# Optimization experiments

Measured on AMD Instinct MI355X. Metric: run time of the kernel, lower is better.

## Reference

```python
import jax, jax.numpy as jnp
import numpy as np

N_NODES = 500000
N_EDGES = 16000000


def setup_inputs() -> dict:
    key = jax.random.key(0)
    ks = jax.random.split(key, 9)
    x = jax.random.normal(ks[0], (N_NODES, 15), dtype=jnp.float32)
    edge_index = jax.random.randint(ks[1], (2, N_EDGES), 0, N_NODES, dtype=jnp.int64)
    batch_index = jax.random.randint(ks[2], (N_NODES,), 0, 64, dtype=jnp.int64)
    def glorot(k, shape):
        lim = (6.0 / (shape[0] + shape[1])) ** 0.5
        return jax.random.uniform(k, shape, jnp.float32, -lim, lim)
    W1 = glorot(ks[3], (15, 15)); b1 = jnp.zeros((15,), jnp.float32)
    W2 = glorot(ks[4], (15, 15)); b2 = jnp.zeros((15,), jnp.float32)
    W3 = glorot(ks[5], (15, 4));  b3 = jnp.zeros((4,), jnp.float32)
    return {"x": x, "edge_index": edge_index, "batch_index": batch_index,
            "W1": W1, "b1": b1, "W2": W2, "b2": b2, "W3": W3, "b3": b3}


def _gcn_conv(x, W, b, src, dst, norm, n):
    # linear transform (tiny GEMM), then normalized scatter-add aggregation
    h = x @ W                                   # [N, out]
    msg = h[src] * norm[:, None]                # [E+N, out] gather + scale
    out = jax.ops.segment_sum(msg, dst, num_segments=n)
    return out + b


def reference(x, edge_index, batch_index, W1, b1, W2, b2, W3, b3):
    n = x.shape[0]
    loops = jnp.arange(n, dtype=edge_index.dtype)
    src = jnp.concatenate([edge_index[0], loops])   # self-loops appended
    dst = jnp.concatenate([edge_index[1], loops])
    # symmetric normalization D^-1/2 A D^-1/2 (deg over targets, incl. self-loops)
    deg = jax.ops.segment_sum(jnp.ones_like(dst, dtype=x.dtype), dst, num_segments=n)
    dis = jnp.where(deg > 0, jax.lax.rsqrt(deg), 0.0)
    norm = dis[src] * dis[dst]                      # [E+N]
    h = jax.nn.relu(_gcn_conv(x, W1, b1, src, dst, norm, n))
    h = jax.nn.relu(_gcn_conv(h, W2, b2, src, dst, norm, n))
    out = _gcn_conv(h, W3, b3, src, dst, norm, n)   # [N, 4]
    return out
```

## Files before the change

### kernel.cpp

```cpp
#include <hip/hip_runtime.h>
#include <hip/hip_fp16.h>


typedef unsigned int uint;
typedef unsigned short ushort;
typedef unsigned long long ull;

#define NBMAX 1024
#define BKN 512
#define BCAP 17408
#define SCAP 24576
#define PT_THREADS 512
#define PT_TILE 8192
#define NPART 8
#define BAR_STRIDE 528
#define BAR_LAYER (7 * BAR_STRIDE)

__global__ void k_init(uint* __restrict__ gcur, uint* __restrict__ bars) {
    int t = threadIdx.x;
    gcur[t] = (uint)t * BCAP;
    for (int i = t; i < 3 * BAR_LAYER; i += 1024) bars[i] = 0;
}

__global__ __launch_bounds__(PT_THREADS) void k_part(const int* __restrict__ src,
                                                     const int* __restrict__ dst, int E,
                                                     uint* __restrict__ gcur,
                                                     uint* __restrict__ bucketed) {
    __shared__ uint stage[PT_TILE];
    __shared__ ushort sbuck[PT_TILE];
    __shared__ uint hist[NBMAX], lofs[NBMAX], base[NBMAX];
    __shared__ uint tsum[PT_THREADS];
    int t = threadIdx.x;
    long long start = (long long)blockIdx.x * PT_TILE;
    int cnt = (int)min((long long)PT_TILE, (long long)E - start);

    hist[2 * t] = 0; hist[2 * t + 1] = 0;
    __syncthreads();
    uint myb[16], myr[16], mys[16];
#pragma unroll
    for (int k = 0; k < 16; ++k) {
        int idx = t + k * PT_THREADS;
        if (idx < cnt) {
            uint d = (uint)dst[start + idx];
            uint s = (uint)src[start + idx];
            uint b = d >> 9;
            myb[k] = b;
            mys[k] = s | ((d & 511u) << 19);
            myr[k] = atomicAdd(&hist[b], 1u);
        }
    }
    __syncthreads();
    uint h0 = hist[2 * t], h1 = hist[2 * t + 1];
    tsum[t] = h0 + h1;
    __syncthreads();
    for (int off = 1; off < PT_THREADS; off <<= 1) {
        uint x = (t >= off) ? tsum[t - off] : 0u;
        __syncthreads();
        tsum[t] += x;
        __syncthreads();
    }
    uint ex = tsum[t] - (h0 + h1);
    lofs[2 * t] = ex;
    lofs[2 * t + 1] = ex + h0;
    if (h0) base[2 * t] = atomicAdd(&gcur[2 * t], h0);
    if (h1) base[2 * t + 1] = atomicAdd(&gcur[2 * t + 1], h1);
    __syncthreads();
#pragma unroll
    for (int k = 0; k < 16; ++k) {
        int idx = t + k * PT_THREADS;
        if (idx < cnt) {
            uint pos = lofs[myb[k]] + myr[k];
            stage[pos] = mys[k];
            sbuck[pos] = (ushort)myb[k];
        }
    }
    __syncthreads();
#pragma unroll
    for (int k = 0; k < 16; ++k) {
        int idx = t + k * PT_THREADS;
        if (idx < cnt) {
            uint b = sbuck[idx];
            uint pos = base[b] + ((uint)idx - lofs[b]);
            if (pos < (uint)(b + 1) * BCAP) bucketed[pos] = stage[idx];
        }
    }
}

__global__ __launch_bounds__(512) void k_csr(const uint* __restrict__ bucketed,
                                             const uint* __restrict__ gcur,
                                             uint* __restrict__ rowp8,
                                             float* __restrict__ dis,
                                             int* __restrict__ srcS, int N) {
    __shared__ uint c[BKN * NPART];
    __shared__ uint tsum[512];
    __shared__ __align__(16) int stage[SCAP];
    int b = blockIdx.x, t = threadIdx.x;
    uint beg = (uint)b * BCAP;
    uint end = min(gcur[b], (uint)(b + 1) * BCAP);
    for (int i = t; i < BKN * NPART; i += 512) c[i] = 0;
    __syncthreads();
    for (uint e = beg + t; e < end; e += 512) {
        uint v = bucketed[e];
        uint key = (((v & 0x7ffffu) >> 16) << 9) | (v >> 19);
        atomicAdd(&c[key], 1u);
    }
    __syncthreads();
    {
        int node = (b << 9) + t;
        if (node < N) {
            uint deg = 0;
#pragma unroll
            for (int p = 0; p < NPART; ++p) deg += c[(p << 9) | t];
            dis[node] = rsqrtf((float)(deg + 1u));
        }
    }
    uint cnt[8], pad[8], ps = 0;
#pragma unroll
    for (int i = 0; i < 8; ++i) {
        cnt[i] = c[t * 8 + i];
        pad[i] = (cnt[i] + 3u) & ~3u;
        ps += pad[i];
    }
    __syncthreads();
    tsum[t] = ps;
    __syncthreads();
    for (int off = 1; off < 512; off <<= 1) {
        uint x = (t >= off) ? tsum[t - off] : 0u;
        __syncthreads();
        tsum[t] += x;
        __syncthreads();
    }
    uint tot = tsum[511];
    uint kb = tsum[t] - ps;
    uint slab = (uint)b * SCAP;
    int p = t >> 6, local0 = (t & 63) << 3;
    uint run = kb;
#pragma unroll
    for (int i = 0; i < 8; ++i) {
        uint st = run;
        rowp8[((uint)p << 19) + (uint)((b << 9) + local0 + i)] =
            (slab + st) | (cnt[i] << 25);
        c[t * 8 + i] = st;
        for (uint q = cnt[i]; q < pad[i]; ++q) {
            uint idx = st + q;
            if (idx < (uint)SCAP) stage[idx] = N;
            else srcS[slab + idx] = N;
        }
        run += pad[i];
    }
    __syncthreads();
    for (uint e = beg + t; e < end; e += 512) {
        uint v = bucketed[e];
        uint s = v & 0x7ffffu;
        uint key = ((s >> 16) << 9) | (v >> 19);
        uint idx = atomicAdd(&c[key], 1u);
        if (idx < (uint)SCAP) stage[idx] = (int)s;
        else srcS[slab + idx] = (int)s;
    }
    __syncthreads();
    uint capped = min(tot, (uint)SCAP);
    uint cap4 = capped & ~3u;
    for (uint i = t * 4; i < cap4; i += 512 * 4)
        *(int4*)(srcS + slab + i) = *(const int4*)(stage + i);
    if (t < (int)(capped & 3u)) srcS[slab + cap4 + t] = stage[cap4 + t];
}

__global__ void k_lin_first(const float* __restrict__ x, const float* __restrict__ W,
                            const float* __restrict__ dis, __half* __restrict__ A, int N) {
    int i = blockIdx.x * blockDim.x + threadIdx.x;
    if (i >= N) return;
    float in[15];
#pragma unroll
    for (int j = 0; j < 15; ++j) in[j] = x[i * 15 + j];
    float di = dis[i];
#pragma unroll
    for (int o = 0; o < 15; ++o) {
        float acc = 0.f;
#pragma unroll
        for (int j = 0; j < 15; ++j) acc = fmaf(in[j], W[j * 15 + o], acc);
        A[i * 16 + o] = __float2half(acc * di);
    }
    A[i * 16 + 15] = __float2half(0.f);
}

__device__ __forceinline__ void softbar(uint* __restrict__ bars, int phase, int nblk) {
    __syncthreads();
    if (threadIdx.x == 0) {
        uint* row = bars + phase * BAR_STRIDE;
        uint ngroups = ((uint)nblk + 31u) >> 5;
        uint g = (uint)blockIdx.x >> 5;
        uint gsz = min(32u, (uint)nblk - g * 32u);
        uint prev = atomicAdd(&row[16 + g * 16], 1u);
        if (prev + 1u == gsz) atomicAdd(&row[0], 1u);
        int spins = 0;
        while (spins < 2000) {
            uint v = __hip_atomic_load(&row[0], __ATOMIC_RELAXED,
                                       __HIP_MEMORY_SCOPE_AGENT);
            if (v >= ngroups) break;
            __builtin_amdgcn_s_sleep(8);
            ++spins;
        }
    }
    __syncthreads();
}

template <int TW>
__device__ __forceinline__ void load_row(const __half* __restrict__ tab, int node,
                                         float (&acc)[TW]) {
    if constexpr (TW == 16) {
        int4 w0 = *(const int4*)(tab + (size_t)node * 16);
        int4 w1 = *(const int4*)(tab + (size_t)node * 16 + 8);
        const __half2* h0 = (const __half2*)&w0;
        const __half2* h1 = (const __half2*)&w1;
#pragma unroll
        for (int u = 0; u < 4; ++u) {
            float2 f0 = __half22float2(h0[u]);
            float2 f1 = __half22float2(h1[u]);
            acc[2 * u] = f0.x;
            acc[2 * u + 1] = f0.y;
            acc[8 + 2 * u] = f1.x;
            acc[8 + 2 * u + 1] = f1.y;
        }
    } else {
        int2 w = *(const int2*)(tab + (size_t)node * 4);
        const __half2* h = (const __half2*)&w;
        float2 f0 = __half22float2(h[0]);
        float2 f1 = __half22float2(h[1]);
        acc[0] = f0.x; acc[1] = f0.y; acc[2] = f1.x; acc[3] = f1.y;
    }
}

template <int TW>
__device__ __forceinline__ void gather_seg(const __half* __restrict__ tab,
                                           const int* __restrict__ srcS,
                                           uint rv, float (&acc)[TW]) {
    uint cnt = rv >> 25;
    if (!cnt) return;
    uint e = rv & 0x1ffffffu;
    uint end4 = e + ((cnt + 3u) & ~3u);
    for (; e < end4; e += 4) {
        int4 s4 = *(const int4*)(srcS + e);
        if constexpr (TW == 16) {
            const int4* p0 = (const int4*)(tab + (size_t)s4.x * 16);
            const int4* p1 = (const int4*)(tab + (size_t)s4.y * 16);
            const int4* p2 = (const int4*)(tab + (size_t)s4.z * 16);
            const int4* p3 = (const int4*)(tab + (size_t)s4.w * 16);
            int4 r[8];
            r[0] = p0[0]; r[1] = p1[0]; r[2] = p2[0]; r[3] = p3[0];
            r[4] = p0[1]; r[5] = p1[1]; r[6] = p2[1]; r[7] = p3[1];
#pragma unroll
            for (int q = 0; q < 8; ++q) {
                const __half2* h2 = (const __half2*)&r[q];
                int base = (q >> 2) * 8;
#pragma unroll
                for (int u = 0; u < 4; ++u) {
                    float2 f = __half22float2(h2[u]);
                    acc[base + 2 * u] += f.x;
                    acc[base + 2 * u + 1] += f.y;
                }
            }
        } else {
            int2 r0 = *(const int2*)(tab + (size_t)s4.x * 4);
            int2 r1 = *(const int2*)(tab + (size_t)s4.y * 4);
            int2 r2 = *(const int2*)(tab + (size_t)s4.z * 4);
            int2 r3 = *(const int2*)(tab + (size_t)s4.w * 4);
            const __half2* h0 = (const __half2*)&r0;
            const __half2* h1 = (const __half2*)&r1;
            const __half2* h2 = (const __half2*)&r2;
            const __half2* h3 = (const __half2*)&r3;
#pragma unroll
            for (int u = 0; u < 2; ++u) {
                float2 f0 = __half22float2(h0[u]);
                float2 f1 = __half22float2(h1[u]);
                float2 f2 = __half22float2(h2[u]);
                float2 f3 = __half22float2(h3[u]);
                acc[2 * u] += (f0.x + f1.x) + (f2.x + f3.x);
                acc[2 * u + 1] += (f0.y + f1.y) + (f2.y + f3.y);
            }
        }
    }
}

template <int L>
__global__ __launch_bounds__(512, 8) void k_pull_res(
    const __half* __restrict__ tab, const int* __restrict__ srcS,
    const uint* __restrict__ rowp8, const float* __restrict__ dis,
    const float* __restrict__ Wm, const float* __restrict__ bias,
    void* __restrict__ outp, uint* __restrict__ bars, int nblk, int N) {
    constexpr int TW = (L == 3) ? 4 : 16;
    __shared__ float wl[240];
    int t = threadIdx.x;
    int node = (blockIdx.x << 9) + t;
    if constexpr (L == 1) {
        for (int i = t; i < 225; i += 512) wl[i] = Wm[i];
        if (t < 15) wl[225 + t] = bias[t];
    }
    if constexpr (L == 2) {
        for (int i = t; i < 60; i += 512) wl[i] = Wm[i];
        if (t < 15) wl[60 + t] = bias[t];
    }
    if constexpr (L == 3) {
        if (t < 4) wl[t] = bias[t];
    }
    __syncthreads();
    bool v = node < N;
    float a[TW];
    if (v) load_row<TW>(tab, node, a);
    uint rv = v ? rowp8[(uint)node] : 0u;
    for (int p = 0; p < NPART; ++p) {
        uint nv = 0u;
        if (p < NPART - 1) {
            uint pb = (uint)(p + 1) << 19;
            if (v) nv = rowp8[pb + (uint)node];
        }
        if (v) gather_seg<TW>(tab, srcS, rv, a);
        if (p < NPART - 1) softbar(bars, p, nblk);
        rv = nv;
    }
    if (!v) return;
    float di = dis[node];
    if constexpr (L == 3) {
        float4 o;
        o.x = a[0] * di + wl[0];
        o.y = a[1] * di + wl[1];
        o.z = a[2] * di + wl[2];
        o.w = a[3] * di + wl[3];
        *(float4*)((float*)outp + (size_t)node * 4) = o;
    } else {
        float h[15];
#pragma unroll
        for (int j = 0; j < 15; ++j) {
            float bj = (L == 1) ? wl[225 + j] : wl[60 + j];
            h[j] = fmaxf(a[j] * di + bj, 0.f);
        }
        if constexpr (L == 1) {
            float o[16];
            o[15] = 0.f;
#pragma unroll
            for (int j = 0; j < 15; ++j) {
                float s = 0.f;
#pragma unroll
                for (int k = 0; k < 15; ++k) s = fmaf(h[k], wl[k * 15 + j], s);
                o[j] = s * di;
            }
            __half2 ob[8];
#pragma unroll
            for (int j = 0; j < 8; ++j)
                ob[j] = __floats2half2_rn(o[2 * j], o[2 * j + 1]);
            *(int4*)((__half*)outp + (size_t)node * 16) = *(int4*)&ob[0];
            *(int4*)((__half*)outp + (size_t)node * 16 + 8) = *(int4*)&ob[4];
        } else {
            float o[4];
#pragma unroll
            for (int j = 0; j < 4; ++j) {
                float s = 0.f;
#pragma unroll
                for (int k = 0; k < 15; ++k) s = fmaf(h[k], wl[k * 4 + j], s);
                o[j] = s * di;
            }
            __half2 ob[2];
            ob[0] = __floats2half2_rn(o[0], o[1]);
            ob[1] = __floats2half2_rn(o[2], o[3]);
            *(float2*)((__half*)outp + (size_t)node * 4) = *(float2*)&ob[0];
        }
    }
}

extern "C" void kernel_launch(void* const* d_in, const int* in_sizes, int n_in,
                              void* d_out, int out_size, void* d_ws, size_t ws_size,
                              hipStream_t stream) {
    const float* x  = (const float*)d_in[0];
    const int*   ei = (const int*)d_in[1];
    const float* W1 = (const float*)d_in[3];
    const float* b1 = (const float*)d_in[4];
    const float* W2 = (const float*)d_in[5];
    const float* b2 = (const float*)d_in[6];
    const float* W3 = (const float*)d_in[7];
    const float* b3 = (const float*)d_in[8];
    float* out = (float*)d_out;

    const int N = in_sizes[0] / 15;
    const int E = in_sizes[1] / 2;
    const int* src = ei;
    const int* dst = ei + E;
    const int NBr = (N + BKN - 1) / BKN;
    const int PB  = NBr;

    char* ws = (char*)d_ws;
    auto align = [](size_t v) { return (v + 255) & ~(size_t)255; };
    size_t off = 0;
    uint* rowp8 = (uint*)(ws + off); off += align((size_t)NPART * (1u << 19) * 4);
    float* dis  = (float*)(ws + off); off += align((size_t)N * 4);
    uint* gcur  = (uint*)(ws + off); off += align((size_t)NBMAX * 4);
    uint* bars  = (uint*)(ws + off); off += align((size_t)3 * BAR_LAYER * 4);
    int*  srcS  = (int*)(ws + off);  off += align((size_t)NBMAX * SCAP * 4);
    char* slabY = ws + off;
    uint*   bucketed = (uint*)slabY;
    __half* Bp = (__half*)slabY;
    __half* Cp = (__half*)(slabY + align((size_t)(N + 1) * 16 * 2));
    off += align((size_t)NBMAX * BCAP * 4);
    __half* Ap = (__half*)(ws + off);

    const int nTiles = (E + PT_TILE - 1) / PT_TILE;
    const int nbN = (N + 255) / 256;

    k_init<<<1, 1024, 0, stream>>>(gcur, bars);
    k_part<<<nTiles, PT_THREADS, 0, stream>>>(src, dst, E, gcur, bucketed);
    k_csr<<<NBr, 512, 0, stream>>>(bucketed, gcur, rowp8, dis, srcS, N);

    k_lin_first<<<nbN, 256, 0, stream>>>(x, W1, dis, Ap, N);
    hipMemsetAsync(Ap + (size_t)N * 16, 0, 16 * 2, stream);
    hipMemsetAsync(Bp + (size_t)N * 16, 0, 16 * 2, stream);
    hipMemsetAsync(Cp + (size_t)N * 4, 0, 4 * 2, stream);

    k_pull_res<1><<<PB, 512, 0, stream>>>(Ap, srcS, rowp8, dis, W2, b1, Bp,
                                          bars + 0 * BAR_LAYER, PB, N);
    k_pull_res<2><<<PB, 512, 0, stream>>>(Bp, srcS, rowp8, dis, W3, b2, Cp,
                                          bars + 1 * BAR_LAYER, PB, N);
    k_pull_res<3><<<PB, 512, 0, stream>>>(Cp, srcS, rowp8, dis, nullptr, b3, out,
                                          bars + 2 * BAR_LAYER, PB, N);
}
```

Baseline: 928.5 us.

## Split 16-wide gather rows across thread pairs, recombine via shared memory

For layers 1 and 2, each thread now gathers one 8-half slice of the feature row for two nodes instead of the full 16-half row for one node, so thread pairs cooperate on a node. The two slices are staged in a padded shared-memory tile and recombined before the dense transform. This cuts per-thread registers and spreads the memory-level parallelism differently across lanes. In exchange it adds a 34 KB shared buffer, which may limit occupancy, plus an extra block barrier.

After: 926.7 us. Within noise of the previous version (-0.2%).

```diff
diff --git a/kernel.cpp b/kernel.cpp
--- a/kernel.cpp
+++ b/kernel.cpp
@@ -204,79 +204,72 @@
     __syncthreads();
 }
 
-template <int TW>
-__device__ __forceinline__ void load_row(const __half* __restrict__ tab, int node,
-                                         float (&acc)[TW]) {
-    if constexpr (TW == 16) {
-        int4 w0 = *(const int4*)(tab + (size_t)node * 16);
-        int4 w1 = *(const int4*)(tab + (size_t)node * 16 + 8);
-        const __half2* h0 = (const __half2*)&w0;
-        const __half2* h1 = (const __half2*)&w1;
-#pragma unroll
-        for (int u = 0; u < 4; ++u) {
-            float2 f0 = __half22float2(h0[u]);
-            float2 f1 = __half22float2(h1[u]);
-            acc[2 * u] = f0.x;
-            acc[2 * u + 1] = f0.y;
-            acc[8 + 2 * u] = f1.x;
-            acc[8 + 2 * u + 1] = f1.y;
-        }
-    } else {
-        int2 w = *(const int2*)(tab + (size_t)node * 4);
-        const __half2* h = (const __half2*)&w;
-        float2 f0 = __half22float2(h[0]);
-        float2 f1 = __half22float2(h[1]);
-        acc[0] = f0.x; acc[1] = f0.y; acc[2] = f1.x; acc[3] = f1.y;
-    }
-}
-
-template <int TW>
-__device__ __forceinline__ void gather_seg(const __half* __restrict__ tab,
-                                           const int* __restrict__ srcS,
-                                           uint rv, float (&acc)[TW]) {
+__device__ __forceinline__ void load_half(const __half* __restrict__ tab, int node,
+                                          int j2, float (&acc)[8]) {
+    int4 w = *(const int4*)(tab + (size_t)node * 16 + j2 * 8);
+    const __half2* h = (const __half2*)&w;
+#pragma unroll
+    for (int u = 0; u < 4; ++u) {
+        float2 f = __half22float2(h[u]);
+        acc[2 * u] = f.x;
+        acc[2 * u + 1] = f.y;
+    }
+}
+
+__device__ __forceinline__ void gather_half(const __half* __restrict__ tab,
+                                            const int* __restrict__ srcS,
+                                            uint rv, int j2, float (&acc)[8]) {
     uint cnt = rv >> 25;
     if (!cnt) return;
     uint e = rv & 0x1ffffffu;
     uint end4 = e + ((cnt + 3u) & ~3u);
     for (; e < end4; e += 4) {
         int4 s4 = *(const int4*)(srcS + e);
-        if constexpr (TW == 16) {
-            const int4* p0 = (const int4*)(tab + (size_t)s4.x * 16);
-            const int4* p1 = (const int4*)(tab + (size_t)s4.y * 16);
-            const int4* p2 = (const int4*)(tab + (size_t)s4.z * 16);
-            const int4* p3 = (const int4*)(tab + (size_t)s4.w * 16);
-            int4 r[8];
-            r[0] = p0[0]; r[1] = p1[0]; r[2] = p2[0]; r[3] = p3[0];
-            r[4] = p0[1]; r[5] = p1[1]; r[6] = p2[1]; r[7] = p3[1];
-#pragma unroll
-            for (int q = 0; q < 8; ++q) {
-                const __half2* h2 = (const __half2*)&r[q];
-                int base = (q >> 2) * 8;
-#pragma unroll
-                for (int u = 0; u < 4; ++u) {
-                    float2 f = __half22float2(h2[u]);
-                    acc[base + 2 * u] += f.x;
-                    acc[base + 2 * u + 1] += f.y;
-                }
-            }
-        } else {
-            int2 r0 = *(const int2*)(tab + (size_t)s4.x * 4);
-            int2 r1 = *(const int2*)(tab + (size_t)s4.y * 4);
-            int2 r2 = *(const int2*)(tab + (size_t)s4.z * 4);
-            int2 r3 = *(const int2*)(tab + (size_t)s4.w * 4);
-            const __half2* h0 = (const __half2*)&r0;
-            const __half2* h1 = (const __half2*)&r1;
-            const __half2* h2 = (const __half2*)&r2;
-            const __half2* h3 = (const __half2*)&r3;
-#pragma unroll
-            for (int u = 0; u < 2; ++u) {
-                float2 f0 = __half22float2(h0[u]);
-                float2 f1 = __half22float2(h1[u]);
-                float2 f2 = __half22float2(h2[u]);
-                float2 f3 = __half22float2(h3[u]);
-                acc[2 * u] += (f0.x + f1.x) + (f2.x + f3.x);
-                acc[2 * u + 1] += (f0.y + f1.y) + (f2.y + f3.y);
-            }
+        int4 r0 = *(const int4*)(tab + (size_t)s4.x * 16 + j2 * 8);
+        int4 r1 = *(const int4*)(tab + (size_t)s4.y * 16 + j2 * 8);
+        int4 r2 = *(const int4*)(tab + (size_t)s4.z * 16 + j2 * 8);
+        int4 r3 = *(const int4*)(tab + (size_t)s4.w * 16 + j2 * 8);
+        const __half2* h0 = (const __half2*)&r0;
+        const __half2* h1 = (const __half2*)&r1;
+        const __half2* h2 = (const __half2*)&r2;
+        const __half2* h3 = (const __half2*)&r3;
+#pragma unroll
+        for (int u = 0; u < 4; ++u) {
+            float2 f0 = __half22float2(h0[u]);
+            float2 f1 = __half22float2(h1[u]);
+            float2 f2 = __half22float2(h2[u]);
+            float2 f3 = __half22float2(h3[u]);
+            acc[2 * u] += (f0.x + f1.x) + (f2.x + f3.x);
+            acc[2 * u + 1] += (f0.y + f1.y) + (f2.y + f3.y);
+        }
+    }
+}
+
+__device__ __forceinline__ void gather_row4(const __half* __restrict__ tab,
+                                            const int* __restrict__ srcS,
+                                            uint rv, float (&acc)[4]) {
+    uint cnt = rv >> 25;
+    if (!cnt) return;
+    uint e = rv & 0x1ffffffu;
+    uint end4 = e + ((cnt + 3u) & ~3u);
+    for (; e < end4; e += 4) {
+        int4 s4 = *(const int4*)(srcS + e);
+        int2 r0 = *(const int2*)(tab + (size_t)s4.x * 4);
+        int2 r1 = *(const int2*)(tab + (size_t)s4.y * 4);
+        int2 r2 = *(const int2*)(tab + (size_t)s4.z * 4);
+        int2 r3 = *(const int2*)(tab + (size_t)s4.w * 4);
+        const __half2* h0 = (const __half2*)&r0;
+        const __half2* h1 = (const __half2*)&r1;
+        const __half2* h2 = (const __half2*)&r2;
+        const __half2* h3 = (const __half2*)&r3;
+#pragma unroll
+        for (int u = 0; u < 2; ++u) {
+            float2 f0 = __half22float2(h0[u]);
+            float2 f1 = __half22float2(h1[u]);
+            float2 f2 = __half22float2(h2[u]);
+            float2 f3 = __half22float2(h3[u]);
+            acc[2 * u] += (f0.x + f1.x) + (f2.x + f3.x);
+            acc[2 * u + 1] += (f0.y + f1.y) + (f2.y + f3.y);
         }
     }
 }
@@ -287,39 +280,34 @@
     const uint* __restrict__ rowp8, const float* __restrict__ dis,
     const float* __restrict__ Wm, const float* __restrict__ bias,
     void* __restrict__ outp, uint* __restrict__ bars, int nblk, int N) {
-    constexpr int TW = (L == 3) ? 4 : 16;
-    __shared__ float wl[240];
     int t = threadIdx.x;
-    int node = (blockIdx.x << 9) + t;
-    if constexpr (L == 1) {
-        for (int i = t; i < 225; i += 512) wl[i] = Wm[i];
-        if (t < 15) wl[225 + t] = bias[t];
-    }
-    if constexpr (L == 2) {
-        for (int i = t; i < 60; i += 512) wl[i] = Wm[i];
-        if (t < 15) wl[60 + t] = bias[t];
-    }
     if constexpr (L == 3) {
+        __shared__ float wl[4];
+        int node = (blockIdx.x << 9) + t;
         if (t < 4) wl[t] = bias[t];
-    }
-    __syncthreads();
-    bool v = node < N;
-    float a[TW];
-    if (v) load_row<TW>(tab, node, a);
-    uint rv = v ? rowp8[(uint)node] : 0u;
-    for (int p = 0; p < NPART; ++p) {
-        uint nv = 0u;
-        if (p < NPART - 1) {
-            uint pb = (uint)(p + 1) << 19;
-            if (v) nv = rowp8[pb + (uint)node];
-        }
-        if (v) gather_seg<TW>(tab, srcS, rv, a);
-        if (p < NPART - 1) softbar(bars, p, nblk);
-        rv = nv;
-    }
-    if (!v) return;
-    float di = dis[node];
-    if constexpr (L == 3) {
+        __syncthreads();
+        bool v = node < N;
+        float a[4];
+        if (v) {
+            int2 w = *(const int2*)(tab + (size_t)node * 4);
+            const __half2* h = (const __half2*)&w;
+            float2 f0 = __half22float2(h[0]);
+            float2 f1 = __half22float2(h[1]);
+            a[0] = f0.x; a[1] = f0.y; a[2] = f1.x; a[3] = f1.y;
+        }
+        uint rv = v ? rowp8[(uint)node] : 0u;
+        for (int p = 0; p < NPART; ++p) {
+            uint nv = 0u;
+            if (p < NPART - 1) {
+                uint pb = (uint)(p + 1) << 19;
+                if (v) nv = rowp8[pb + (uint)node];
+            }
+            if (v) gather_row4(tab, srcS, rv, a);
+            if (p < NPART - 1) softbar(bars, p, nblk);
+            rv = nv;
+        }
+        if (!v) return;
+        float di = dis[node];
         float4 o;
         o.x = a[0] * di + wl[0];
         o.y = a[1] * di + wl[1];
@@ -327,11 +315,54 @@
         o.w = a[3] * di + wl[3];
         *(float4*)((float*)outp + (size_t)node * 4) = o;
     } else {
+        __shared__ float wl[240];
+        __shared__ float sh[512 * 17];
+        int pr = t >> 1, j2 = t & 1;
+        int base = blockIdx.x << 9;
+        int nA = base + pr, nB = base + 256 + pr;
+        if constexpr (L == 1) {
+            for (int i = t; i < 225; i += 512) wl[i] = Wm[i];
+            if (t < 15) wl[225 + t] = bias[t];
+        } else {
+            for (int i = t; i < 60; i += 512) wl[i] = Wm[i];
+            if (t < 15) wl[60 + t] = bias[t];
+        }
+        __syncthreads();
+        bool vA = nA < N, vB = nB < N;
+        float aA[8], aB[8];
+        if (vA) load_half(tab, nA, j2, aA);
+        if (vB) load_half(tab, nB, j2, aB);
+        uint rvA = vA ? rowp8[(uint)nA] : 0u;
+        uint rvB = vB ? rowp8[(uint)nB] : 0u;
+        for (int p = 0; p < NPART; ++p) {
+            uint nvA = 0u, nvB = 0u;
+            if (p < NPART - 1) {
+                uint pb = (uint)(p + 1) << 19;
+                if (vA) nvA = rowp8[pb + (uint)nA];
+                if (vB) nvB = rowp8[pb + (uint)nB];
+            }
+            if (vA) gather_half(tab, srcS, rvA, j2, aA);
+            if (vB) gather_half(tab, srcS, rvB, j2, aB);
+            if (p < NPART - 1) softbar(bars, p, nblk);
+            rvA = nvA; rvB = nvB;
+        }
+        if (vA) {
+#pragma unroll
+            for (int u = 0; u < 8; ++u) sh[pr * 17 + j2 * 8 + u] = aA[u];
+        }
+        if (vB) {
+#pragma unroll
+            for (int u = 0; u < 8; ++u) sh[(256 + pr) * 17 + j2 * 8 + u] = aB[u];
+        }
+        __syncthreads();
+        int node = base + t;
+        if (node >= N) return;
+        float di = dis[node];
         float h[15];
 #pragma unroll
         for (int j = 0; j < 15; ++j) {
             float bj = (L == 1) ? wl[225 + j] : wl[60 + j];
-            h[j] = fmaxf(a[j] * di + bj, 0.f);
+            h[j] = fmaxf(sh[t * 17 + j] * di + bj, 0.f);
         }
         if constexpr (L == 1) {
             float o[16];
```
